# Performance work log

Hardware: AMD Instinct MI355X
Metric: run time of the kernel (lower is better)

Reference implementation:

```python
import jax, jax.numpy as jnp
import numpy as np

D_MODEL = 512
H = 8
D_K = D_MODEL // H


def setup_inputs() -> dict:
    key = jax.random.key(0)
    ks = jax.random.split(key, 11)
    B, S = 2, 2048
    scale = 1.0 / np.sqrt(D_MODEL)
    return {
        "q": jax.random.normal(ks[0], (B, S, D_MODEL), jnp.float32),
        "v": jax.random.normal(ks[1], (B, S, D_MODEL), jnp.float32),
        "k": jax.random.normal(ks[2], (B, S, D_MODEL), jnp.float32),
        "w_q": jax.random.normal(ks[3], (D_MODEL, D_MODEL), jnp.float32) * scale,
        "b_q": jnp.zeros((D_MODEL,), jnp.float32),
        "w_k": jax.random.normal(ks[4], (D_MODEL, D_MODEL), jnp.float32) * scale,
        "b_k": jnp.zeros((D_MODEL,), jnp.float32),
        "w_v": jax.random.normal(ks[5], (D_MODEL, D_MODEL), jnp.float32) * scale,
        "b_v": jnp.zeros((D_MODEL,), jnp.float32),
        "w_o": jax.random.normal(ks[6], (D_MODEL, D_MODEL), jnp.float32) * scale,
        "b_o": jnp.zeros((D_MODEL,), jnp.float32),
    }


def reference(q, v, k, w_q, b_q, w_k, b_k, w_v, b_v, w_o, b_o):
    B, S, _ = q.shape
    # projections (nn.Linear: x @ W.T + b)
    query = q @ w_q.T + b_q
    key_t = k @ w_k.T + b_k
    value = v @ w_v.T + b_v
    # split heads: [B, S, H, D_K] -> [B, H, S, D_K]
    query = query.reshape(B, S, H, D_K).transpose(0, 2, 1, 3)
    key_t = key_t.reshape(B, S, H, D_K).transpose(0, 2, 1, 3)
    value = value.reshape(B, S, H, D_K).transpose(0, 2, 1, 3)
    # unfused attention: full [B, H, S, S] score matrix
    scores = jnp.einsum("bhqd,bhkd->bhqk", query, key_t) / jnp.sqrt(
        jnp.asarray(D_K, query.dtype)
    )
    attn = jax.nn.softmax(scores, axis=-1)  # dropout inactive in eval
    x = jnp.einsum("bhqk,bhkd->bhqd", attn, value)
    # merge heads and output projection
    x = x.transpose(0, 2, 1, 3).reshape(B, S, D_MODEL)
    return x @ w_o.T + b_o
```

## Files before the change

kernel.cpp:

```cpp
#include <hip/hip_runtime.h>
#include <hip/hip_bf16.h>


typedef __attribute__((ext_vector_type(8))) short short8;
typedef __attribute__((ext_vector_type(4))) short short4v;
typedef __attribute__((ext_vector_type(4))) float f32x4;
typedef __attribute__((ext_vector_type(4))) unsigned int uint4v;

#define DM 512
#define SEQ 2048
#define NROW 4096
#define LOG2E 1.44269504088896341f
#define MFMA(a, b, c) __builtin_amdgcn_mfma_f32_16x16x32_bf16(a, b, c, 0, 0, 0)
#define FENCE() __asm__ __volatile__("" ::: "memory")

#if __has_builtin(__builtin_amdgcn_exp2f)
#define EXP2(x) __builtin_amdgcn_exp2f(x)
#else
#define EXP2(x) exp2f(x)
#endif

__device__ __forceinline__ float bf_bits2f(short s) {
    unsigned int u = ((unsigned int)(unsigned short)s) << 16;
    return __builtin_bit_cast(float, u);
}
__device__ __forceinline__ short f2bf_r(float f) {
    unsigned int u = __builtin_bit_cast(unsigned int, f) + 0x8000u;
    return (short)(u >> 16);
}
__device__ __forceinline__ unsigned int pack_bf16(float lo, float hi) {
    unsigned int ul = __builtin_bit_cast(unsigned int, lo) + 0x8000u;
    unsigned int uh = __builtin_bit_cast(unsigned int, hi) + 0x8000u;
    return __builtin_amdgcn_perm(uh, ul, 0x07060302u);
}

__device__ __forceinline__ void gload_lds16(const void* src, void* lds_dst) {
    __builtin_amdgcn_global_load_lds(
        (const __attribute__((address_space(1))) unsigned int*)src,
        (__attribute__((address_space(3))) unsigned int*)lds_dst, 16, 0, 0);
}

template <int ROWS, int NW, int SH = 0>
__device__ __forceinline__ void stage_tile(const short* __restrict__ gsrc, size_t gstride,
                                           short* lds, int wave, int lane) {
    constexpr int ISSUES = ROWS * 8 / (64 * NW);
    #pragma unroll
    for (int i = 0; i < ISSUES; i++) {
        const int blk = i * NW + wave;
        const int g = blk * 64 + lane;
        const int row = g >> 3;
        const int cb = (g & 7) ^ ((row >> SH) & 7);
        gload_lds16(gsrc + (size_t)row * gstride + cb * 8, lds + (size_t)blk * 512);
    }
}

__device__ __forceinline__ bool detect_f32(const unsigned int* __restrict__ q, int* cnt_lds) {
    if (threadIdx.x == 0) *cnt_lds = 0;
    __syncthreads();
    int local = 0;
    for (int i = threadIdx.x; i < 1024; i += blockDim.x) {
        unsigned int lo = q[i] & 0x7FFFu;
        if (lo >= 0x3000u && lo < 0x4400u) local++;
    }
    if (local) atomicAdd(cnt_lds, local);
    __syncthreads();
    return *cnt_lds < 512;
}

struct ConvArgs { const void* src[11]; short* dst[11]; int n[11]; int* flag; };
__global__ void convert_all(ConvArgs a) {
    __shared__ int cnt;
    const bool f32m = detect_f32((const unsigned int*)a.src[0], &cnt);
    if (threadIdx.x == 0) *a.flag = f32m ? 1 : 0;
    const int tid = blockIdx.x * 256 + threadIdx.x;
    const int stride = gridDim.x * 256;
    if (f32m) {
        for (int s = 0; s < 11; s++) {
            const float4* sp = (const float4*)a.src[s];
            short4v* dp = (short4v*)a.dst[s];
            const int n4 = a.n[s] >> 2;
            for (int i = tid; i < n4; i += stride) {
                float4 v = sp[i];
                short4v o;
                o[0] = f2bf_r(v.x); o[1] = f2bf_r(v.y);
                o[2] = f2bf_r(v.z); o[3] = f2bf_r(v.w);
                dp[i] = o;
            }
        }
    } else {
        for (int s = 0; s < 11; s++) {
            const short4v* sp = (const short4v*)a.src[s];
            short4v* dp = (short4v*)a.dst[s];
            const int n4 = a.n[s] >> 2;
            for (int i = tid; i < n4; i += stride) dp[i] = sp[i];
        }
    }
}

template <int MT, int NT>
__device__ __forceinline__ void gemm_core(const short* __restrict__ A,
                                          const short* __restrict__ W,
                                          int m0, int n0, short* Alds, short* Blds,
                                          int wave, int lane,
                                          f32x4 (&acc)[MT / 64][NT / 16]) {
    const int rc = lane & 15, quad = lane >> 4;
    const short* Ag = A + (size_t)m0 * DM;
    const short* Bg = W + (size_t)n0 * DM;
    constexpr int ABUF = MT * 64, BBUF = NT * 64;
    constexpr int INFLIGHT = (MT + NT) * 8 / 256;
    constexpr int NITER = DM / 64;

    stage_tile<MT, 4>(Ag, DM, Alds, wave, lane);
    stage_tile<NT, 4>(Bg, DM, Blds, wave, lane);

    for (int i = 0; i < NITER; i++) {
        const int cur = i & 1;
        const short* Ac = Alds + cur * ABUF;
        const short* Bc = Blds + cur * BBUF;
        if (i + 1 < NITER) {
            stage_tile<MT, 4>(Ag + (i + 1) * 64, DM, Alds + (cur ^ 1) * ABUF, wave, lane);
            stage_tile<NT, 4>(Bg + (i + 1) * 64, DM, Blds + (cur ^ 1) * BBUF, wave, lane);
            __builtin_amdgcn_s_waitcnt(0x3F70 | INFLIGHT);
        } else {
            __builtin_amdgcn_s_waitcnt(0x3F70);
        }
        FENCE();
        __builtin_amdgcn_s_barrier();
        FENCE();
        #pragma unroll
        for (int h = 0; h < 2; h++) {
            short8 bf[NT / 16];
            #pragma unroll
            for (int nt = 0; nt < NT / 16; nt++) {
                const int br = nt * 16 + rc;
                bf[nt] = *(const short8*)&Bc[br * 64 + (((quad + 4 * h) ^ (br & 7)) * 8)];
            }
            #pragma unroll
            for (int ms = 0; ms < MT / 64; ms++) {
                const int ar = wave * (MT / 4) + ms * 16 + rc;
                short8 af = *(const short8*)&Ac[ar * 64 + (((quad + 4 * h) ^ (ar & 7)) * 8)];
                #pragma unroll
                for (int nt = 0; nt < NT / 16; nt++)
                    acc[ms][nt] = MFMA(af, bf[nt], acc[ms][nt]);
            }
        }
        FENCE();
        __builtin_amdgcn_s_barrier();
        FENCE();
    }
}

struct QKVArgs {
    const short* A[3]; const short* W[3]; const short* Bi[3];
    short* Cq; short* Ck; short* Cv;
};
__global__ __launch_bounds__(256, 2) void qkv_gemm(QKVArgs args) {
    __shared__ __align__(16) short Alds[2][128 * 64];
    __shared__ __align__(16) short Blds[2][128 * 64];
    const int z = blockIdx.z;
    const int wave = threadIdx.x >> 6, lane = threadIdx.x & 63;
    const int rc = lane & 15, quad = lane >> 4;
    const int m0 = blockIdx.x * 128, n0 = blockIdx.y * 128;

    f32x4 acc[2][8] = {};
    gemm_core<128, 128>(args.A[z], args.W[z], m0, n0, &Alds[0][0], &Blds[0][0], wave, lane, acc);
    const short* bias = args.Bi[z];

    if (z == 2) {
        #pragma unroll
        for (int ms = 0; ms < 2; ms++) {
            const int mw = m0 + wave * 32 + ms * 16;
            const int b = mw >> 11, sb = (mw & 2047) + quad * 4;
            #pragma unroll
            for (int nt = 0; nt < 8; nt++) {
                const int dg = n0 + nt * 16 + rc;
                const int hh = dg >> 6, dd = dg & 63;
                const float bv = bf_bits2f(bias[dg]);
                short4v pk;
                #pragma unroll
                for (int r = 0; r < 4; r++) pk[r] = f2bf_r(acc[ms][nt][r] + bv);
                *(short4v*)(args.Cv + ((size_t)((b * 8 + hh) * 64 + dd)) * SEQ + sb) = pk;
            }
        }
    } else {
        short* C = (z == 0) ? args.Cq : args.Ck;
        const float sc = (z == 0) ? (0.125f * LOG2E) : 1.0f;
        #pragma unroll
        for (int ms = 0; ms < 2; ms++) {
            const int mw = m0 + wave * 32 + ms * 16;
            #pragma unroll
            for (int r = 0; r < 4; r++) {
                int mrow = mw + quad * 4 + r;
                if (z == 1) {
                    const int u = mrow & 63;
                    mrow = (mrow & ~63) |
                           (16 * ((u >> 3) & 3) + 4 * (u & 3) + 2 * (u >> 5) + ((u >> 2) & 1));
                }
                #pragma unroll
                for (int nt = 0; nt < 8; nt++) {
                    const int col = n0 + nt * 16 + rc;
                    const float bv = bf_bits2f(bias[col]);
                    C[(size_t)mrow * DM + col] = f2bf_r((acc[ms][nt][r] + bv) * sc);
                }
            }
        }
    }
}

__global__ __launch_bounds__(256, 4) void out_gemm(
    const short* __restrict__ A, const short* __restrict__ W,
    const short* __restrict__ bias, void* __restrict__ Cout,
    const int* __restrict__ dtf) {
    __shared__ __align__(16) short Alds[2][64 * 64];
    __shared__ __align__(16) short Blds[2][64 * 64];
    const bool f32out = (*dtf != 0);
    const int wave = threadIdx.x >> 6, lane = threadIdx.x & 63;
    const int rc = lane & 15, quad = lane >> 4;
    const int m0 = blockIdx.x * 64, n0 = blockIdx.y * 64;
    f32x4 acc[1][4] = {};
    gemm_core<64, 64>(A, W, m0, n0, &Alds[0][0], &Blds[0][0], wave, lane, acc);
    const int mw = m0 + wave * 16;
    #pragma unroll
    for (int nt = 0; nt < 4; nt++) {
        const int col = n0 + nt * 16 + rc;
        const float bv = bf_bits2f(bias[col]);
        #pragma unroll
        for (int r = 0; r < 4; r++) {
            const size_t idx = (size_t)(mw + quad * 4 + r) * DM + col;
            const float val = acc[0][nt][r] + bv;
            if (f32out) ((float*)Cout)[idx] = val;
            else        ((short*)Cout)[idx] = f2bf_r(val);
        }
    }
}

__global__ __launch_bounds__(256, 2) void attn_kernel(
    const short* __restrict__ Q, const short* __restrict__ K,
    const short* __restrict__ Vt, short* __restrict__ X)
{
    __shared__ __align__(16) short Klds[2][128 * 64];
    __shared__ __align__(16) short Vlds[2][2][64 * 64];

    const int wave = threadIdx.x >> 6, lane = threadIdx.x & 63;
    const int rc = lane & 15, quad = lane >> 4;
    const int qh = wave & 1, kh = wave >> 1;
    const int L = blockIdx.x;
    const int bh = (L & 7) * 2 + ((L >> 3) >> 5);
    const int qb = (L >> 3) & 31;
    const size_t baseQK = (size_t)(bh >> 3) * SEQ * DM + (size_t)(bh & 7) * 64;
    const short* Qb = Q + baseQK;
    const short* Kb = K + baseQK;
    const short* Vb = Vt + (size_t)bh * 64 * SEQ;
    const int q0 = qb * 64 + qh * 32;

    short8 qa[2][2];
    #pragma unroll
    for (int ms = 0; ms < 2; ms++)
        #pragma unroll
        for (int h = 0; h < 2; h++)
            qa[ms][h] = *(const short8*)(Qb + (size_t)(q0 + ms * 16 + rc) * DM + h * 32 + quad * 8);

    short8 ones;
    #pragma unroll
    for (int j = 0; j < 8; j++) ones[j] = (short)0x3F80;

    f32x4 o[4][2] = {};
    f32x4 lsum[2] = {};

    int koff[4][2], voff[4][2];
    #pragma unroll
    for (int kt = 0; kt < 4; kt++) {
        const int row = kh * 64 + rc * 4 + kt;
        #pragma unroll
        for (int h = 0; h < 2; h++)
            koff[kt][h] = row * 64 + (((quad + 4 * h) ^ ((row >> 2) & 7)) * 8);
    }
    #pragma unroll
    for (int dt = 0; dt < 4; dt++) {
        const int row = dt * 16 + rc;
        #pragma unroll
        for (int h = 0; h < 2; h++)
            voff[dt][h] = row * 64 + (((quad + 4 * h) ^ (row & 7)) * 8);
    }

    stage_tile<128, 4, 2>(Kb, DM, &Klds[0][0], wave, lane);
    stage_tile<64, 4>(Vb, SEQ, &Vlds[0][0][0], wave, lane);
    stage_tile<64, 4>(Vb + 64, SEQ, &Vlds[0][1][0], wave, lane);
    __syncthreads();

    for (int it = 0; it < 16; ++it) {
        const int cur = it & 1;
        if (it + 1 < 16) {
            const int k0n = (it + 1) * 128;
            stage_tile<128, 4, 2>(Kb + (size_t)k0n * DM, DM, &Klds[cur ^ 1][0], wave, lane);
            stage_tile<64, 4>(Vb + k0n, SEQ, &Vlds[cur ^ 1][0][0], wave, lane);
            stage_tile<64, 4>(Vb + k0n + 64, SEQ, &Vlds[cur ^ 1][1][0], wave, lane);
        }

        const short* Kt = &Klds[cur][0];
        const short* Vl = &Vlds[cur][kh][0];

        short8 kf[4][2];
        #pragma unroll
        for (int kt = 0; kt < 4; kt++)
            #pragma unroll
            for (int h = 0; h < 2; h++)
                kf[kt][h] = *(const short8*)&Kt[koff[kt][h]];
        f32x4 s[2][4];
        __builtin_amdgcn_s_setprio(1);
        #pragma unroll
        for (int ms = 0; ms < 2; ms++)
            #pragma unroll
            for (int kt = 0; kt < 4; kt++) {
                f32x4 t = {};
                t = MFMA(kf[kt][0], qa[ms][0], t);
                t = MFMA(kf[kt][1], qa[ms][1], t);
                s[ms][kt] = t;
            }
        __builtin_amdgcn_s_setprio(0);
        short8 pa[2][2];
        #pragma unroll
        for (int ms = 0; ms < 2; ms++)
            #pragma unroll
            for (int h = 0; h < 2; h++) {
                uint4v w;
                w[0] = pack_bf16(EXP2(s[ms][2 * h][0]), EXP2(s[ms][2 * h][1]));
                w[1] = pack_bf16(EXP2(s[ms][2 * h][2]), EXP2(s[ms][2 * h][3]));
                w[2] = pack_bf16(EXP2(s[ms][2 * h + 1][0]), EXP2(s[ms][2 * h + 1][1]));
                w[3] = pack_bf16(EXP2(s[ms][2 * h + 1][2]), EXP2(s[ms][2 * h + 1][3]));
                pa[ms][h] = __builtin_bit_cast(short8, w);
            }
        __builtin_amdgcn_s_setprio(1);
        #pragma unroll
        for (int ms = 0; ms < 2; ms++) {
            lsum[ms] = MFMA(ones, pa[ms][0], lsum[ms]);
            lsum[ms] = MFMA(ones, pa[ms][1], lsum[ms]);
        }
        #pragma unroll
        for (int dt = 0; dt < 4; dt++) {
            short8 v0 = *(const short8*)&Vl[voff[dt][0]];
            short8 v1 = *(const short8*)&Vl[voff[dt][1]];
            #pragma unroll
            for (int ms = 0; ms < 2; ms++) {
                o[dt][ms] = MFMA(v0, pa[ms][0], o[dt][ms]);
                o[dt][ms] = MFMA(v1, pa[ms][1], o[dt][ms]);
            }
        }
        __builtin_amdgcn_s_setprio(0);
        __syncthreads();
    }

    float* OM = (float*)&Klds[0][0];
    float* LM = (float*)&Vlds[0][0][0];
    if (kh == 1) {
        #pragma unroll
        for (int dt = 0; dt < 4; dt++)
            #pragma unroll
            for (int ms = 0; ms < 2; ms++)
                *(f32x4*)&OM[(((dt * 2 + ms) * 2 + qh) * 64 + lane) * 4] = o[dt][ms];
        #pragma unroll
        for (int ms = 0; ms < 2; ms++)
            LM[(qh * 2 + ms) * 64 + lane] = lsum[ms][0];
    }
    __syncthreads();
    if (kh == 0) {
        short* Xr = X + baseQK;
        #pragma unroll
        for (int ms = 0; ms < 2; ms++) {
            const float inv = 1.0f / (lsum[ms][0] + LM[(qh * 2 + ms) * 64 + lane]);
            const size_t rowoff = (size_t)(q0 + ms * 16 + rc) * DM;
            #pragma unroll
            for (int dt = 0; dt < 4; dt++) {
                const f32x4 op = *(const f32x4*)&OM[(((dt * 2 + ms) * 2 + qh) * 64 + lane) * 4];
                short4v pk;
                #pragma unroll
                for (int r = 0; r < 4; r++) pk[r] = f2bf_r((o[dt][ms][r] + op[r]) * inv);
                *(short4v*)(Xr + rowoff + dt * 16 + quad * 4) = pk;
            }
        }
    }
}

extern "C" void kernel_launch(void* const* d_in, const int* in_sizes, int n_in,
                              void* d_out, int out_size, void* d_ws, size_t ws_size,
                              hipStream_t stream) {
    char* ws = (char*)d_ws;
    const size_t SEQB = (size_t)NROW * DM * sizeof(short);
    const size_t WB   = (size_t)DM * DM * sizeof(short);
    const size_t BB   = (size_t)DM * sizeof(short);

    size_t off = 0;
    short* qc = (short*)(ws + off); off += SEQB;
    short* vc = (short*)(ws + off); off += SEQB;
    short* kc = (short*)(ws + off); off += SEQB;
    short* wq = (short*)(ws + off); off += WB;
    short* wk = (short*)(ws + off); off += WB;
    short* wv = (short*)(ws + off); off += WB;
    short* wo = (short*)(ws + off); off += WB;
    short* bq = (short*)(ws + off); off += BB;
    short* bk = (short*)(ws + off); off += BB;
    short* bv = (short*)(ws + off); off += BB;
    short* bo = (short*)(ws + off); off += BB;
    off = (off + 255) & ~(size_t)255;
    short* Qp  = (short*)(ws + off); off += SEQB;
    short* Kp  = (short*)(ws + off); off += SEQB;
    short* Vtp = (short*)(ws + off); off += SEQB;
    short* Xp  = (short*)(ws + off); off += SEQB;
    int*   dtf = (int*)(ws + off);  off += 256;

    ConvArgs ca;
    const void* srcs[11] = {d_in[0], d_in[1], d_in[2], d_in[3], d_in[5], d_in[7],
                            d_in[9], d_in[4], d_in[6], d_in[8], d_in[10]};
    short* dsts[11] = {qc, vc, kc, wq, wk, wv, wo, bq, bk, bv, bo};
    int ns[11] = {NROW * DM, NROW * DM, NROW * DM, DM * DM, DM * DM, DM * DM,
                  DM * DM, DM, DM, DM, DM};
    for (int i = 0; i < 11; i++) { ca.src[i] = srcs[i]; ca.dst[i] = dsts[i]; ca.n[i] = ns[i]; }
    ca.flag = dtf;
    convert_all<<<1024, 256, 0, stream>>>(ca);

    QKVArgs qa;
    qa.A[0] = qc; qa.A[1] = kc; qa.A[2] = vc;
    qa.W[0] = wq; qa.W[1] = wk; qa.W[2] = wv;
    qa.Bi[0] = bq; qa.Bi[1] = bk; qa.Bi[2] = bv;
    qa.Cq = Qp; qa.Ck = Kp; qa.Cv = Vtp;
    qkv_gemm<<<dim3(NROW / 128, DM / 128, 3), 256, 0, stream>>>(qa);

    attn_kernel<<<dim3(512), 256, 0, stream>>>(Qp, Kp, Vtp, Xp);

    out_gemm<<<dim3(NROW / 64, DM / 64), 256, 0, stream>>>(
        Xp, wo, bo, d_out, dtf);
}
```

Measured before the change: 146.1 us.

## Split attention key tile across four wave pairs with 512-thread blocks

The attention kernel now runs 8 waves per block instead of 4. Each key-split group handles 32 keys of the 128-key tile rather than 64, and the partial outputs and row sums from three groups are reduced through shared memory at the end. The K row permutation in the QKV projection is removed and the K LDS layout and swizzle are adjusted to match. The aim is more waves in flight to hide latency, paid for with a larger cross-wave reduction and half-size MFMA chunks per wave.

```diff
diff --git a/kernel.cpp b/kernel.cpp
--- a/kernel.cpp
+++ b/kernel.cpp
@@ -189,19 +189,12 @@
         for (int ms = 0; ms < 2; ms++) {
             const int mw = m0 + wave * 32 + ms * 16;
             #pragma unroll
-            for (int r = 0; r < 4; r++) {
-                int mrow = mw + quad * 4 + r;
-                if (z == 1) {
-                    const int u = mrow & 63;
-                    mrow = (mrow & ~63) |
-                           (16 * ((u >> 3) & 3) + 4 * (u & 3) + 2 * (u >> 5) + ((u >> 2) & 1));
-                }
+            for (int nt = 0; nt < 8; nt++) {
+                const int col = n0 + nt * 16 + rc;
+                const float bv = bf_bits2f(bias[col]);
                 #pragma unroll
-                for (int nt = 0; nt < 8; nt++) {
-                    const int col = n0 + nt * 16 + rc;
-                    const float bv = bf_bits2f(bias[col]);
-                    C[(size_t)mrow * DM + col] = f2bf_r((acc[ms][nt][r] + bv) * sc);
-                }
+                for (int r = 0; r < 4; r++)
+                    C[(size_t)(mw + quad * 4 + r) * DM + col] = f2bf_r((acc[ms][nt][r] + bv) * sc);
             }
         }
     }
@@ -234,12 +227,11 @@
     }
 }
 
-__global__ __launch_bounds__(256, 2) void attn_kernel(
+__global__ __launch_bounds__(512, 4) void attn_kernel(
     const short* __restrict__ Q, const short* __restrict__ K,
     const short* __restrict__ Vt, short* __restrict__ X)
 {
-    __shared__ __align__(16) short Klds[2][128 * 64];
-    __shared__ __align__(16) short Vlds[2][2][64 * 64];
+    __shared__ __align__(16) short S[2][16384];
 
     const int wave = threadIdx.x >> 6, lane = threadIdx.x & 63;
     const int rc = lane & 15, quad = lane >> 4;
@@ -267,114 +259,116 @@
     f32x4 o[4][2] = {};
     f32x4 lsum[2] = {};
 
-    int koff[4][2], voff[4][2];
-    #pragma unroll
-    for (int kt = 0; kt < 4; kt++) {
-        const int row = kh * 64 + rc * 4 + kt;
+    int koff[2][2], voff[4];
+    #pragma unroll
+    for (int kt = 0; kt < 2; kt++) {
+        const int row = kh * 32 + rc * 2 + kt;
         #pragma unroll
         for (int h = 0; h < 2; h++)
-            koff[kt][h] = row * 64 + (((quad + 4 * h) ^ ((row >> 2) & 7)) * 8);
+            koff[kt][h] = row * 64 + (((quad + 4 * h) ^ ((row >> 1) & 7)) * 8);
     }
     #pragma unroll
     for (int dt = 0; dt < 4; dt++) {
         const int row = dt * 16 + rc;
-        #pragma unroll
-        for (int h = 0; h < 2; h++)
-            voff[dt][h] = row * 64 + (((quad + 4 * h) ^ (row & 7)) * 8);
-    }
-
-    stage_tile<128, 4, 2>(Kb, DM, &Klds[0][0], wave, lane);
-    stage_tile<64, 4>(Vb, SEQ, &Vlds[0][0][0], wave, lane);
-    stage_tile<64, 4>(Vb + 64, SEQ, &Vlds[0][1][0], wave, lane);
+        voff[dt] = row * 64 + ((((kh & 1) * 4 + quad) ^ (row & 7)) * 8);
+    }
+
+    stage_tile<128, 8, 1>(Kb, DM, &S[0][0], wave, lane);
+    stage_tile<64, 8>(Vb, SEQ, &S[0][8192], wave, lane);
+    stage_tile<64, 8>(Vb + 64, SEQ, &S[0][12288], wave, lane);
     __syncthreads();
 
     for (int it = 0; it < 16; ++it) {
         const int cur = it & 1;
         if (it + 1 < 16) {
             const int k0n = (it + 1) * 128;
-            stage_tile<128, 4, 2>(Kb + (size_t)k0n * DM, DM, &Klds[cur ^ 1][0], wave, lane);
-            stage_tile<64, 4>(Vb + k0n, SEQ, &Vlds[cur ^ 1][0][0], wave, lane);
-            stage_tile<64, 4>(Vb + k0n + 64, SEQ, &Vlds[cur ^ 1][1][0], wave, lane);
-        }
-
-        const short* Kt = &Klds[cur][0];
-        const short* Vl = &Vlds[cur][kh][0];
-
-        short8 kf[4][2];
-        #pragma unroll
-        for (int kt = 0; kt < 4; kt++)
+            stage_tile<128, 8, 1>(Kb + (size_t)k0n * DM, DM, &S[cur ^ 1][0], wave, lane);
+            stage_tile<64, 8>(Vb + k0n, SEQ, &S[cur ^ 1][8192], wave, lane);
+            stage_tile<64, 8>(Vb + k0n + 64, SEQ, &S[cur ^ 1][12288], wave, lane);
+        }
+
+        const short* Kt = &S[cur][0];
+        const short* Vl = &S[cur][8192 + (kh >> 1) * 4096];
+
+        short8 kf[2][2];
+        #pragma unroll
+        for (int kt = 0; kt < 2; kt++)
             #pragma unroll
             for (int h = 0; h < 2; h++)
                 kf[kt][h] = *(const short8*)&Kt[koff[kt][h]];
-        f32x4 s[2][4];
+        f32x4 s[2][2];
         __builtin_amdgcn_s_setprio(1);
         #pragma unroll
         for (int ms = 0; ms < 2; ms++)
             #pragma unroll
-            for (int kt = 0; kt < 4; kt++) {
+            for (int kt = 0; kt < 2; kt++) {
                 f32x4 t = {};
                 t = MFMA(kf[kt][0], qa[ms][0], t);
                 t = MFMA(kf[kt][1], qa[ms][1], t);
                 s[ms][kt] = t;
             }
         __builtin_amdgcn_s_setprio(0);
-        short8 pa[2][2];
+        short8 pa[2];
+        #pragma unroll
+        for (int ms = 0; ms < 2; ms++) {
+            uint4v w;
+            #pragma unroll
+            for (int r = 0; r < 4; r++)
+                w[r] = pack_bf16(EXP2(s[ms][0][r]), EXP2(s[ms][1][r]));
+            pa[ms] = __builtin_bit_cast(short8, w);
+        }
+        __builtin_amdgcn_s_setprio(1);
         #pragma unroll
         for (int ms = 0; ms < 2; ms++)
-            #pragma unroll
-            for (int h = 0; h < 2; h++) {
-                uint4v w;
-                w[0] = pack_bf16(EXP2(s[ms][2 * h][0]), EXP2(s[ms][2 * h][1]));
-                w[1] = pack_bf16(EXP2(s[ms][2 * h][2]), EXP2(s[ms][2 * h][3]));
-                w[2] = pack_bf16(EXP2(s[ms][2 * h + 1][0]), EXP2(s[ms][2 * h + 1][1]));
-                w[3] = pack_bf16(EXP2(s[ms][2 * h + 1][2]), EXP2(s[ms][2 * h + 1][3]));
-                pa[ms][h] = __builtin_bit_cast(short8, w);
-            }
-        __builtin_amdgcn_s_setprio(1);
-        #pragma unroll
-        for (int ms = 0; ms < 2; ms++) {
-            lsum[ms] = MFMA(ones, pa[ms][0], lsum[ms]);
-            lsum[ms] = MFMA(ones, pa[ms][1], lsum[ms]);
-        }
+            lsum[ms] = MFMA(ones, pa[ms], lsum[ms]);
         #pragma unroll
         for (int dt = 0; dt < 4; dt++) {
-            short8 v0 = *(const short8*)&Vl[voff[dt][0]];
-            short8 v1 = *(const short8*)&Vl[voff[dt][1]];
-            #pragma unroll
-            for (int ms = 0; ms < 2; ms++) {
-                o[dt][ms] = MFMA(v0, pa[ms][0], o[dt][ms]);
-                o[dt][ms] = MFMA(v1, pa[ms][1], o[dt][ms]);
-            }
+            short8 v = *(const short8*)&Vl[voff[dt]];
+            #pragma unroll
+            for (int ms = 0; ms < 2; ms++)
+                o[dt][ms] = MFMA(v, pa[ms], o[dt][ms]);
         }
         __builtin_amdgcn_s_setprio(0);
         __syncthreads();
     }
 
-    float* OM = (float*)&Klds[0][0];
-    float* LM = (float*)&Vlds[0][0][0];
-    if (kh == 1) {
+    float* OM = (float*)&S[0][0];
+    float* LM = OM + 12288;
+    if (kh > 0) {
         #pragma unroll
         for (int dt = 0; dt < 4; dt++)
             #pragma unroll
-            for (int ms = 0; ms < 2; ms++)
-                *(f32x4*)&OM[(((dt * 2 + ms) * 2 + qh) * 64 + lane) * 4] = o[dt][ms];
+            for (int ms = 0; ms < 2; ms++) {
+                const int e = (kh - 1) * 16 + (dt * 2 + ms) * 2 + qh;
+                *(f32x4*)&OM[(e * 64 + lane) * 4] = o[dt][ms];
+            }
         #pragma unroll
         for (int ms = 0; ms < 2; ms++)
-            LM[(qh * 2 + ms) * 64 + lane] = lsum[ms][0];
+            LM[((kh - 1) * 4 + qh * 2 + ms) * 64 + lane] = lsum[ms][0];
     }
     __syncthreads();
     if (kh == 0) {
         short* Xr = X + baseQK;
         #pragma unroll
         for (int ms = 0; ms < 2; ms++) {
-            const float inv = 1.0f / (lsum[ms][0] + LM[(qh * 2 + ms) * 64 + lane]);
+            float l = lsum[ms][0];
+            #pragma unroll
+            for (int p = 0; p < 3; p++) l += LM[(p * 4 + qh * 2 + ms) * 64 + lane];
+            const float inv = 1.0f / l;
             const size_t rowoff = (size_t)(q0 + ms * 16 + rc) * DM;
             #pragma unroll
             for (int dt = 0; dt < 4; dt++) {
-                const f32x4 op = *(const f32x4*)&OM[(((dt * 2 + ms) * 2 + qh) * 64 + lane) * 4];
+                f32x4 acc = o[dt][ms];
+                #pragma unroll
+                for (int p = 0; p < 3; p++) {
+                    const int e = p * 16 + (dt * 2 + ms) * 2 + qh;
+                    const f32x4 op = *(const f32x4*)&OM[(e * 64 + lane) * 4];
+                    #pragma unroll
+                    for (int r = 0; r < 4; r++) acc[r] += op[r];
+                }
                 short4v pk;
                 #pragma unroll
-                for (int r = 0; r < 4; r++) pk[r] = f2bf_r((o[dt][ms][r] + op[r]) * inv);
+                for (int r = 0; r < 4; r++) pk[r] = f2bf_r(acc[r] * inv);
                 *(short4v*)(Xr + rowoff + dt * 16 + quad * 4) = pk;
             }
         }
@@ -425,7 +419,7 @@
     qa.Cq = Qp; qa.Ck = Kp; qa.Cv = Vtp;
     qkv_gemm<<<dim3(NROW / 128, DM / 128, 3), 256, 0, stream>>>(qa);
 
-    attn_kernel<<<dim3(512), 256, 0, stream>>>(Qp, Kp, Vtp, Xp);
+    attn_kernel<<<dim3(512), 512, 0, stream>>>(Qp, Kp, Vtp, Xp);
 
     out_gemm<<<dim3(NROW / 64, DM / 64), 256, 0, stream>>>(
         Xp, wo, bo, d_out, dtf);
```

Measured after the change: 140.8 us. 3.6% less time.
